# Performance work log

Hardware: AMD Instinct MI355X
Metric: run time of the kernel (lower is better)

## Reference

```python
import math
import jax, jax.numpy as jnp
import numpy as np

BS, T, D_MODEL, H = 4, 1024, 1024, 16
D_K = D_MODEL // H


def setup_inputs() -> dict:
    key = jax.random.key(0)
    ks = jax.random.split(key, 16)
    s = 0.02  # weight init scale
    return {
        "q": jax.random.normal(ks[0], (BS, T, D_MODEL), jnp.float32),
        "k": jax.random.normal(ks[1], (BS, T, D_MODEL), jnp.float32),
        "v": jax.random.normal(ks[2], (BS, T, D_MODEL), jnp.float32),
        "pos_emb": jax.random.normal(ks[3], (1, T, D_MODEL), jnp.float32),
        "mask": jnp.ones((BS, T, T), jnp.int32),
        "Wq": jax.random.normal(ks[4], (D_MODEL, D_MODEL), jnp.float32) * s,
        "bq": jax.random.normal(ks[5], (D_MODEL,), jnp.float32) * s,
        "Wk": jax.random.normal(ks[6], (D_MODEL, D_MODEL), jnp.float32) * s,
        "bk": jax.random.normal(ks[7], (D_MODEL,), jnp.float32) * s,
        "Wv": jax.random.normal(ks[8], (D_MODEL, D_MODEL), jnp.float32) * s,
        "bv": jax.random.normal(ks[9], (D_MODEL,), jnp.float32) * s,
        "Wp": jax.random.normal(ks[10], (D_MODEL, D_MODEL), jnp.float32) * s,
        "pos_bias_u": jax.random.normal(ks[11], (H, D_K), jnp.float32) * s,
        "pos_bias_v": jax.random.normal(ks[12], (H, D_K), jnp.float32) * s,
        "Wo": jax.random.normal(ks[13], (D_MODEL, D_MODEL), jnp.float32) * s,
        "bo": jax.random.normal(ks[14], (D_MODEL,), jnp.float32) * s,
    }


def rel_shift(x):
    # x: [b, h, T, P]; Transformer-XL relative shift via pad+reshape
    b, h, t, p = x.shape
    x = jnp.pad(x, ((0, 0), (0, 0), (0, 0), (1, 0)))  # [b,h,T,P+1]
    x = x.reshape(b, h, p + 1, t)[:, :, 1:, :]
    return x.reshape(b, h, t, p)


def reference(q, k, v, pos_emb, mask, Wq, bq, Wk, bk, Wv, bv, Wp,
              pos_bias_u, pos_bias_v, Wo, bo):
    bs, t, d_model = q.shape
    h, d_k = pos_bias_u.shape
    # projections (torch Linear: x @ W.T + b)
    qh = (q @ Wq.T + bq).reshape(bs, t, h, d_k)                      # [b,t,h,d]
    kh = (k @ Wk.T + bk).reshape(bs, t, h, d_k).transpose(0, 2, 1, 3)  # [b,h,s,d]
    vh = (v @ Wv.T + bv).reshape(bs, t, h, d_k).transpose(0, 2, 1, 3)  # [b,h,s,d]
    p = (pos_emb @ Wp.T).reshape(pos_emb.shape[0], -1, h, d_k).transpose(0, 2, 1, 3)  # [1,h,P,d]
    q_u = (qh + pos_bias_u).transpose(0, 2, 1, 3)  # [b,h,t,d]
    q_v = (qh + pos_bias_v).transpose(0, 2, 1, 3)  # [b,h,t,d]
    matrix_ac = jnp.einsum('bhtd,bhsd->bhts', q_u, kh)
    matrix_bd = jnp.einsum('bhtd,hpd->bhtp', q_v, p[0])
    matrix_bd = rel_shift(matrix_bd)
    scores = (matrix_ac + matrix_bd) / math.sqrt(d_k)
    m = mask[:, None, :, :]  # broadcast over heads
    attn = jax.nn.softmax(jnp.where(m == 0, jnp.float32(-10000.0), scores), axis=-1)
    out_h = jnp.einsum('bhts,bhsd->bhtd', attn, vh)
    concat = out_h.transpose(0, 2, 1, 3).reshape(bs, t, d_model)
    output = concat @ Wo.T + bo
    return (output, attn)
```

## Files before the change

### kernel.cpp

```cpp
#include <hip/hip_runtime.h>

typedef _Float16 f16;
typedef __attribute__((ext_vector_type(8))) _Float16 f16x8;
typedef __attribute__((ext_vector_type(4))) float f32x4;

#define LDK 40


__device__ __forceinline__ void stage_f32(const float* __restrict__ src, int ld, f16* dst) {
    int t = threadIdx.x;
    int row = t >> 2;
    int c0 = (t & 3) * 8;
    const float* p = src + (size_t)row * ld + c0;
    float4 u = *(const float4*)p;
    float4 w = *(const float4*)(p + 4);
    f16x8 h;
    h[0] = (f16)u.x; h[1] = (f16)u.y; h[2] = (f16)u.z; h[3] = (f16)u.w;
    h[4] = (f16)w.x; h[5] = (f16)w.y; h[6] = (f16)w.z; h[7] = (f16)w.w;
    *(f16x8*)(dst + row * LDK + c0) = h;
}

__device__ __forceinline__ void stage_f16g(const f16* __restrict__ src, int ld, f16* dst) {
    int t = threadIdx.x;
    int row = t >> 2;
    int c0 = (t & 3) * 8;
    *(f16x8*)(dst + row * LDK + c0) = *(const f16x8*)(src + (size_t)row * ld + c0);
}

__device__ __forceinline__ void stage_vT(const f16* __restrict__ src, f16* dst) {
    int t = threadIdx.x;
    int s = t >> 3;
    int d0 = (t & 7) * 8;
    f16x8 h = *(const f16x8*)(src + (size_t)s * 64 + d0);
#pragma unroll
    for (int j = 0; j < 8; ++j) dst[(d0 + j) * LDK + s] = h[j];
}


__device__ __forceinline__ void mma_step(const f16* As, const f16* Bs, int m_off, int n_off,
                                         f32x4 acc[2][2]) {
    int lane = threadIdx.x & 63;
    int r = lane & 15;
    int kq = (lane >> 4) * 8;
    f16x8 a0 = *(const f16x8*)(As + (m_off + r) * LDK + kq);
    f16x8 a1 = *(const f16x8*)(As + (m_off + 16 + r) * LDK + kq);
    f16x8 b0 = *(const f16x8*)(Bs + (n_off + r) * LDK + kq);
    f16x8 b1 = *(const f16x8*)(Bs + (n_off + 16 + r) * LDK + kq);
    acc[0][0] = __builtin_amdgcn_mfma_f32_16x16x32_f16(a0, b0, acc[0][0], 0, 0, 0);
    acc[0][1] = __builtin_amdgcn_mfma_f32_16x16x32_f16(a0, b1, acc[0][1], 0, 0, 0);
    acc[1][0] = __builtin_amdgcn_mfma_f32_16x16x32_f16(a1, b0, acc[1][0], 0, 0, 0);
    acc[1][1] = __builtin_amdgcn_mfma_f32_16x16x32_f16(a1, b1, acc[1][1], 0, 0, 0);
}

#define GEMM_PROLOGUE()                                         \
    __shared__ f16 As[64 * LDK];                                \
    __shared__ f16 Bs[64 * LDK];                                \
    const int w = threadIdx.x >> 6;                             \
    const int m_off = (w & 1) * 32, n_off = (w >> 1) * 32;      \
    const int lane = threadIdx.x & 63;                          \
    f32x4 zero = {0.f, 0.f, 0.f, 0.f};                          \
    f32x4 acc[2][2] = {{zero, zero}, {zero, zero}};

template <int MODE>
__global__ __launch_bounds__(256) void proj_gemm(
    const float* __restrict__ A, const float* __restrict__ W,
    const float* __restrict__ bias, const float* __restrict__ pbu,
    const float* __restrict__ pbv, f16* __restrict__ o1, f16* __restrict__ o2) {
    GEMM_PROLOGUE();
    const int m0 = blockIdx.y * 64;
    const int n0 = blockIdx.x * 64;
    for (int k0 = 0; k0 < 1024; k0 += 32) {
        stage_f32(A + (size_t)m0 * 1024 + k0, 1024, As);
        stage_f32(W + (size_t)n0 * 1024 + k0, 1024, Bs);
        __syncthreads();
        mma_step(As, Bs, m_off, n_off, acc);
        __syncthreads();
    }
#pragma unroll
    for (int mt = 0; mt < 2; ++mt)
#pragma unroll
        for (int nt = 0; nt < 2; ++nt)
#pragma unroll
            for (int rr = 0; rr < 4; ++rr) {
                int m = m0 + m_off + mt * 16 + (lane >> 4) * 4 + rr;
                int n = n0 + n_off + nt * 16 + (lane & 15);
                float vv = acc[mt][nt][rr];
                if (MODE == 2) {
                    int h = n >> 6, d = n & 63;
                    o1[((size_t)h * 1024 + m) * 64 + d] = (f16)vv;
                } else {
                    float base = vv + bias[n];
                    int b = m >> 10, t = m & 1023, h = n >> 6, d = n & 63;
                    size_t idx = ((size_t)((b * 16 + h) * 1024 + t)) * 64 + d;
                    if (MODE == 0) {
                        o1[idx] = (f16)(base + pbu[n]);
                        o2[idx] = (f16)(base + pbv[n]);
                    } else {
                        o1[idx] = (f16)base;
                    }
                }
            }
}

__global__ __launch_bounds__(256) void bd_gemm(const f16* __restrict__ qv,
                                               const f16* __restrict__ p,
                                               f16* __restrict__ bds) {
    GEMM_PROLOGUE();
    const int bh = blockIdx.z;
    const int h = bh & 15;
    const int m0 = blockIdx.y * 64, n0 = blockIdx.x * 64;
    const f16* Ab = qv + (size_t)bh * 65536;
    const f16* Bb = p + (size_t)h * 65536;
    for (int k0 = 0; k0 < 64; k0 += 32) {
        stage_f16g(Ab + (size_t)m0 * 64 + k0, 64, As);
        stage_f16g(Bb + (size_t)n0 * 64 + k0, 64, Bs);
        __syncthreads();
        mma_step(As, Bs, m_off, n_off, acc);
        __syncthreads();
    }
    f16* B0 = bds + (size_t)bh * 1048576;
#pragma unroll
    for (int mt = 0; mt < 2; ++mt)
#pragma unroll
        for (int nt = 0; nt < 2; ++nt)
#pragma unroll
            for (int rr = 0; rr < 4; ++rr) {
                int r = m0 + m_off + mt * 16 + (lane >> 4) * 4 + rr;
                int c = n0 + n_off + nt * 16 + (lane & 15);
                float vv = acc[mt][nt][rr];
                if (c >= 1023 - r) {
                    B0[(size_t)r * 1024 + (c + r - 1023)] = (f16)vv;
                } else if (r >= 1) {
                    B0[(size_t)(r - 1) * 1024 + (c + r + 1)] = (f16)vv;
                }
            }
}

__global__ __launch_bounds__(256) void ac_gemm(const f16* __restrict__ qu,
                                               const f16* __restrict__ kh,
                                               f16* __restrict__ bds) {
    GEMM_PROLOGUE();
    const int bh = blockIdx.z;
    const int m0 = blockIdx.y * 64, n0 = blockIdx.x * 64;
    const f16* Ab = qu + (size_t)bh * 65536;
    const f16* Bb = kh + (size_t)bh * 65536;
    for (int k0 = 0; k0 < 64; k0 += 32) {
        stage_f16g(Ab + (size_t)m0 * 64 + k0, 64, As);
        stage_f16g(Bb + (size_t)n0 * 64 + k0, 64, Bs);
        __syncthreads();
        mma_step(As, Bs, m_off, n_off, acc);
        __syncthreads();
    }
#pragma unroll
    for (int mt = 0; mt < 2; ++mt)
#pragma unroll
        for (int nt = 0; nt < 2; ++nt)
#pragma unroll
            for (int rr = 0; rr < 4; ++rr) {
                int i = m0 + m_off + mt * 16 + (lane >> 4) * 4 + rr;
                int j = n0 + n_off + nt * 16 + (lane & 15);
                size_t idx = (size_t)bh * 1048576 + (size_t)i * 1024 + j;
                float bdv = (j == i + 1) ? 0.f : (float)bds[idx];
                bds[idx] = (f16)((acc[mt][nt][rr] + bdv) * 0.125f);
            }
}

__global__ __launch_bounds__(256) void softmax_k(const f16* __restrict__ sp,
                                                 const int* __restrict__ mask,
                                                 float* __restrict__ attn) {
    const int row = blockIdx.x;
    const int bh = row >> 10, t = row & 1023;
    const int b = bh >> 4;
    const f16* s = sp + (size_t)row * 1024;
    const int* mk = mask + ((size_t)b * 1024 + t) * 1024;
    const int tid = threadIdx.x;
    float vals[4];
    float mx = -1e30f;
#pragma unroll
    for (int ii = 0; ii < 4; ++ii) {
        int c = tid + ii * 256;
        float v = (float)s[c];
        if (mk[c] == 0) v = -10000.0f;
        vals[ii] = v;
        mx = fmaxf(mx, v);
    }
#pragma unroll
    for (int off = 32; off > 0; off >>= 1) mx = fmaxf(mx, __shfl_xor(mx, off));
    __shared__ float red[4], red2[4];
    if ((tid & 63) == 0) red[tid >> 6] = mx;
    __syncthreads();
    mx = fmaxf(fmaxf(red[0], red[1]), fmaxf(red[2], red[3]));
    float sum = 0.f, e[4];
#pragma unroll
    for (int ii = 0; ii < 4; ++ii) {
        e[ii] = __expf(vals[ii] - mx);
        sum += e[ii];
    }
#pragma unroll
    for (int off = 32; off > 0; off >>= 1) sum += __shfl_xor(sum, off);
    if ((tid & 63) == 0) red2[tid >> 6] = sum;
    __syncthreads();
    sum = red2[0] + red2[1] + red2[2] + red2[3];
    float inv = 1.f / sum;
    float* arow = attn + (size_t)row * 1024;
#pragma unroll
    for (int ii = 0; ii < 4; ++ii) arow[tid + ii * 256] = e[ii] * inv;
}

__global__ __launch_bounds__(256) void pv_gemm(const float* __restrict__ attn,
                                               const f16* __restrict__ vh,
                                               f16* __restrict__ oh) {
    GEMM_PROLOGUE();
    const int bh = blockIdx.z;
    const int b = bh >> 4, h = bh & 15;
    const int m0 = blockIdx.y * 64;
    const float* Ab = attn + (size_t)bh * 1048576;
    const f16* Bb = vh + (size_t)bh * 65536;
    for (int k0 = 0; k0 < 1024; k0 += 32) {
        stage_f32(Ab + (size_t)m0 * 1024 + k0, 1024, As);
        stage_vT(Bb + (size_t)k0 * 64, Bs);
        __syncthreads();
        mma_step(As, Bs, m_off, n_off, acc);
        __syncthreads();
    }
#pragma unroll
    for (int mt = 0; mt < 2; ++mt)
#pragma unroll
        for (int nt = 0; nt < 2; ++nt)
#pragma unroll
            for (int rr = 0; rr < 4; ++rr) {
                int t = m0 + m_off + mt * 16 + (lane >> 4) * 4 + rr;
                int d = n_off + nt * 16 + (lane & 15);
                oh[((size_t)(b * 1024 + t)) * 1024 + h * 64 + d] =
                    (f16)acc[mt][nt][rr];
            }
}

__global__ __launch_bounds__(256) void out_gemm(const f16* __restrict__ A,
                                                const float* __restrict__ W,
                                                const float* __restrict__ bias,
                                                float* __restrict__ out) {
    GEMM_PROLOGUE();
    const int m0 = blockIdx.y * 64;
    const int n0 = blockIdx.x * 64;
    for (int k0 = 0; k0 < 1024; k0 += 32) {
        stage_f16g(A + (size_t)m0 * 1024 + k0, 1024, As);
        stage_f32(W + (size_t)n0 * 1024 + k0, 1024, Bs);
        __syncthreads();
        mma_step(As, Bs, m_off, n_off, acc);
        __syncthreads();
    }
#pragma unroll
    for (int mt = 0; mt < 2; ++mt)
#pragma unroll
        for (int nt = 0; nt < 2; ++nt)
#pragma unroll
            for (int rr = 0; rr < 4; ++rr) {
                int m = m0 + m_off + mt * 16 + (lane >> 4) * 4 + rr;
                int n = n0 + n_off + nt * 16 + (lane & 15);
                out[(size_t)m * 1024 + n] = acc[mt][nt][rr] + bias[n];
            }
}

extern "C" void kernel_launch(void* const* d_in, const int* in_sizes, int n_in,
                              void* d_out, int out_size, void* d_ws, size_t ws_size,
                              hipStream_t stream) {
    (void)in_sizes; (void)n_in; (void)out_size; (void)ws_size;
    const float* q   = (const float*)d_in[0];
    const float* k   = (const float*)d_in[1];
    const float* v   = (const float*)d_in[2];
    const float* pe  = (const float*)d_in[3];
    const int*   msk = (const int*)d_in[4];
    const float* Wq  = (const float*)d_in[5];
    const float* bq  = (const float*)d_in[6];
    const float* Wk  = (const float*)d_in[7];
    const float* bk  = (const float*)d_in[8];
    const float* Wv  = (const float*)d_in[9];
    const float* bv  = (const float*)d_in[10];
    const float* Wp  = (const float*)d_in[11];
    const float* pbu = (const float*)d_in[12];
    const float* pbv = (const float*)d_in[13];
    const float* Wo  = (const float*)d_in[14];
    const float* bo  = (const float*)d_in[15];

    char* ws = (char*)d_ws;
    f16* q_u = (f16*)(ws + 0);
    f16* q_v = (f16*)(ws + 8388608);
    f16* kh  = (f16*)(ws + 16777216);
    f16* vh  = (f16*)(ws + 25165824);
    f16* pp  = (f16*)(ws + 33554432);
    f16* bds = (f16*)(ws + 35651584);
    f16* oh  = (f16*)(ws + 169869312);

    float* out  = (float*)d_out;
    float* attn = out + 4194304;

    dim3 blk(256);
    proj_gemm<0><<<dim3(16, 64), blk, 0, stream>>>(q, Wq, bq, pbu, pbv, q_u, q_v);
    proj_gemm<1><<<dim3(16, 64), blk, 0, stream>>>(k, Wk, bk, nullptr, nullptr, kh, nullptr);
    proj_gemm<1><<<dim3(16, 64), blk, 0, stream>>>(v, Wv, bv, nullptr, nullptr, vh, nullptr);
    proj_gemm<2><<<dim3(16, 16), blk, 0, stream>>>(pe, Wp, nullptr, nullptr, nullptr, pp, nullptr);
    bd_gemm<<<dim3(16, 16, 64), blk, 0, stream>>>(q_v, pp, bds);
    ac_gemm<<<dim3(16, 16, 64), blk, 0, stream>>>(q_u, kh, bds);
    softmax_k<<<dim3(65536), blk, 0, stream>>>(bds, msk, attn);
    pv_gemm<<<dim3(1, 16, 64), blk, 0, stream>>>(attn, vh, oh);
    out_gemm<<<dim3(16, 64), blk, 0, stream>>>(oh, Wo, bo, out);
}
```

Before: 746.0 us.

## Pre-convert inputs to fp16, batch QKV projections, fuse softmax with PV GEMM

A single conversion kernel now turns all fp32 inputs and weights into fp16 once, so the GEMMs stage fp16 directly instead of converting inside every K-loop. The three Q/K/V projections run as one launch over a z dimension. Softmax and the P·V GEMM are merged into one kernel: it computes per-row max and sum, then recomputes the probabilities, writes the fp32 attention output, and feeds fp16 probabilities straight into the MFMA. This removes the re-read of the 256MB fp32 attn tensor. The trade-off is extra conversion traffic, reading the scores twice, and fewer blocks (1024) for the fused kernel.

Result: faster. 703.8 us (-5.6%).

```diff
diff --git a/kernel.cpp b/kernel.cpp
--- a/kernel.cpp
+++ b/kernel.cpp
@@ -6,19 +6,6 @@
 
 #define LDK 40
 
-
-__device__ __forceinline__ void stage_f32(const float* __restrict__ src, int ld, f16* dst) {
-    int t = threadIdx.x;
-    int row = t >> 2;
-    int c0 = (t & 3) * 8;
-    const float* p = src + (size_t)row * ld + c0;
-    float4 u = *(const float4*)p;
-    float4 w = *(const float4*)(p + 4);
-    f16x8 h;
-    h[0] = (f16)u.x; h[1] = (f16)u.y; h[2] = (f16)u.z; h[3] = (f16)u.w;
-    h[4] = (f16)w.x; h[5] = (f16)w.y; h[6] = (f16)w.z; h[7] = (f16)w.w;
-    *(f16x8*)(dst + row * LDK + c0) = h;
-}
 
 __device__ __forceinline__ void stage_f16g(const f16* __restrict__ src, int ld, f16* dst) {
     int t = threadIdx.x;
@@ -61,17 +48,82 @@
     f32x4 zero = {0.f, 0.f, 0.f, 0.f};                          \
     f32x4 acc[2][2] = {{zero, zero}, {zero, zero}};
 
-template <int MODE>
-__global__ __launch_bounds__(256) void proj_gemm(
-    const float* __restrict__ A, const float* __restrict__ W,
-    const float* __restrict__ bias, const float* __restrict__ pbu,
-    const float* __restrict__ pbv, f16* __restrict__ o1, f16* __restrict__ o2) {
+__global__ __launch_bounds__(256) void cvt_all(
+    const float* __restrict__ q, const float* __restrict__ k, const float* __restrict__ v,
+    const float* __restrict__ pe, const float* __restrict__ Wq, const float* __restrict__ Wk,
+    const float* __restrict__ Wv, const float* __restrict__ Wp, const float* __restrict__ Wo,
+    f16* __restrict__ dst) {
+    const int seg = blockIdx.y;
+    const float* srcs[9] = {q, k, v, pe, Wq, Wk, Wv, Wp, Wo};
+    const int sz = (seg < 3) ? 4194304 : 1048576;
+    const size_t off = (seg < 3) ? (size_t)seg * 4194304
+                                 : (size_t)12582912 + (size_t)(seg - 3) * 1048576;
+    const size_t i0 = ((size_t)blockIdx.x * 256 + threadIdx.x) * 16;
+    if (i0 >= (size_t)sz) return;
+    const float* s = srcs[seg] + i0;
+    f16* d = dst + off + i0;
+#pragma unroll
+    for (int half = 0; half < 2; ++half) {
+        float4 u = *(const float4*)(s + half * 8);
+        float4 w = *(const float4*)(s + half * 8 + 4);
+        f16x8 h;
+        h[0] = (f16)u.x; h[1] = (f16)u.y; h[2] = (f16)u.z; h[3] = (f16)u.w;
+        h[4] = (f16)w.x; h[5] = (f16)w.y; h[6] = (f16)w.z; h[7] = (f16)w.w;
+        *(f16x8*)(d + half * 8) = h;
+    }
+}
+
+__global__ __launch_bounds__(256) void proj_qkv(
+    const f16* __restrict__ qf, const f16* __restrict__ kf, const f16* __restrict__ vf,
+    const f16* __restrict__ Wqf, const f16* __restrict__ Wkf, const f16* __restrict__ Wvf,
+    const float* __restrict__ bq, const float* __restrict__ bk, const float* __restrict__ bv,
+    const float* __restrict__ pbu, const float* __restrict__ pbv,
+    f16* __restrict__ q_u, f16* __restrict__ q_v, f16* __restrict__ kh,
+    f16* __restrict__ vh) {
+    GEMM_PROLOGUE();
+    const int z = blockIdx.z;
+    const f16* A = (z == 0) ? qf : (z == 1) ? kf : vf;
+    const f16* W = (z == 0) ? Wqf : (z == 1) ? Wkf : Wvf;
+    const float* bias = (z == 0) ? bq : (z == 1) ? bk : bv;
+    const int m0 = blockIdx.y * 64, n0 = blockIdx.x * 64;
+    for (int k0 = 0; k0 < 1024; k0 += 32) {
+        stage_f16g(A + (size_t)m0 * 1024 + k0, 1024, As);
+        stage_f16g(W + (size_t)n0 * 1024 + k0, 1024, Bs);
+        __syncthreads();
+        mma_step(As, Bs, m_off, n_off, acc);
+        __syncthreads();
+    }
+#pragma unroll
+    for (int mt = 0; mt < 2; ++mt)
+#pragma unroll
+        for (int nt = 0; nt < 2; ++nt)
+#pragma unroll
+            for (int rr = 0; rr < 4; ++rr) {
+                int m = m0 + m_off + mt * 16 + (lane >> 4) * 4 + rr;
+                int n = n0 + n_off + nt * 16 + (lane & 15);
+                float base = acc[mt][nt][rr] + bias[n];
+                int b = m >> 10, t = m & 1023, h = n >> 6, d = n & 63;
+                size_t idx = ((size_t)((b * 16 + h) * 1024 + t)) * 64 + d;
+                if (z == 0) {
+                    q_u[idx] = (f16)(base + pbu[n]);
+                    q_v[idx] = (f16)(base + pbv[n]);
+                } else if (z == 1) {
+                    kh[idx] = (f16)base;
+                } else {
+                    vh[idx] = (f16)base;
+                }
+            }
+}
+
+__global__ __launch_bounds__(256) void proj_p(const f16* __restrict__ A,
+                                              const f16* __restrict__ W,
+                                              f16* __restrict__ o1) {
     GEMM_PROLOGUE();
     const int m0 = blockIdx.y * 64;
     const int n0 = blockIdx.x * 64;
     for (int k0 = 0; k0 < 1024; k0 += 32) {
-        stage_f32(A + (size_t)m0 * 1024 + k0, 1024, As);
-        stage_f32(W + (size_t)n0 * 1024 + k0, 1024, Bs);
+        stage_f16g(A + (size_t)m0 * 1024 + k0, 1024, As);
+        stage_f16g(W + (size_t)n0 * 1024 + k0, 1024, Bs);
         __syncthreads();
         mma_step(As, Bs, m_off, n_off, acc);
         __syncthreads();
@@ -84,21 +136,8 @@
             for (int rr = 0; rr < 4; ++rr) {
                 int m = m0 + m_off + mt * 16 + (lane >> 4) * 4 + rr;
                 int n = n0 + n_off + nt * 16 + (lane & 15);
-                float vv = acc[mt][nt][rr];
-                if (MODE == 2) {
-                    int h = n >> 6, d = n & 63;
-                    o1[((size_t)h * 1024 + m) * 64 + d] = (f16)vv;
-                } else {
-                    float base = vv + bias[n];
-                    int b = m >> 10, t = m & 1023, h = n >> 6, d = n & 63;
-                    size_t idx = ((size_t)((b * 16 + h) * 1024 + t)) * 64 + d;
-                    if (MODE == 0) {
-                        o1[idx] = (f16)(base + pbu[n]);
-                        o2[idx] = (f16)(base + pbv[n]);
-                    } else {
-                        o1[idx] = (f16)base;
-                    }
-                }
+                int h = n >> 6, d = n & 63;
+                o1[((size_t)h * 1024 + m) * 64 + d] = (f16)acc[mt][nt][rr];
             }
 }
 
@@ -165,71 +204,99 @@
             }
 }
 
-__global__ __launch_bounds__(256) void softmax_k(const f16* __restrict__ sp,
-                                                 const int* __restrict__ mask,
-                                                 float* __restrict__ attn) {
-    const int row = blockIdx.x;
-    const int bh = row >> 10, t = row & 1023;
-    const int b = bh >> 4;
-    const f16* s = sp + (size_t)row * 1024;
-    const int* mk = mask + ((size_t)b * 1024 + t) * 1024;
-    const int tid = threadIdx.x;
-    float vals[4];
-    float mx = -1e30f;
-#pragma unroll
-    for (int ii = 0; ii < 4; ++ii) {
-        int c = tid + ii * 256;
-        float v = (float)s[c];
-        if (mk[c] == 0) v = -10000.0f;
-        vals[ii] = v;
-        mx = fmaxf(mx, v);
-    }
-#pragma unroll
-    for (int off = 32; off > 0; off >>= 1) mx = fmaxf(mx, __shfl_xor(mx, off));
-    __shared__ float red[4], red2[4];
-    if ((tid & 63) == 0) red[tid >> 6] = mx;
+__global__ __launch_bounds__(256) void softmax_pv(const f16* __restrict__ scores,
+                                                  const int* __restrict__ mask,
+                                                  const f16* __restrict__ vh,
+                                                  float* __restrict__ attn,
+                                                  f16* __restrict__ oh) {
+    const int bh = blockIdx.y;
+    const int i0 = blockIdx.x * 64;
+    const int b = bh >> 4, h = bh & 15;
+    const f16* S = scores + (size_t)bh * 1048576 + (size_t)i0 * 1024;
+    const int* MK = mask + ((size_t)b * 1024 + i0) * 1024;
+    __shared__ float s_max[64], s_invl[64];
+
+    const int w = threadIdx.x >> 6;
+    const int lane = threadIdx.x & 63;
+
+    for (int rr = 0; rr < 16; ++rr) {
+        int r = w * 16 + rr;
+        const f16* srow = S + (size_t)r * 1024 + lane * 16;
+        const int* mrow = MK + (size_t)r * 1024 + lane * 16;
+        f16x8 a0 = *(const f16x8*)srow;
+        f16x8 a1 = *(const f16x8*)(srow + 8);
+        int4 m0 = *(const int4*)mrow;
+        int4 m1 = *(const int4*)(mrow + 4);
+        int4 m2 = *(const int4*)(mrow + 8);
+        int4 m3 = *(const int4*)(mrow + 12);
+        int mks[16] = {m0.x, m0.y, m0.z, m0.w, m1.x, m1.y, m1.z, m1.w,
+                       m2.x, m2.y, m2.z, m2.w, m3.x, m3.y, m3.z, m3.w};
+        float vals[16];
+        float mx = -1e30f;
+#pragma unroll
+        for (int j = 0; j < 16; ++j) {
+            float v = (j < 8) ? (float)a0[j] : (float)a1[j - 8];
+            if (mks[j] == 0) v = -10000.0f;
+            vals[j] = v;
+            mx = fmaxf(mx, v);
+        }
+#pragma unroll
+        for (int off = 32; off > 0; off >>= 1) mx = fmaxf(mx, __shfl_xor(mx, off));
+        float sum = 0.f;
+#pragma unroll
+        for (int j = 0; j < 16; ++j) sum += __expf(vals[j] - mx);
+#pragma unroll
+        for (int off = 32; off > 0; off >>= 1) sum += __shfl_xor(sum, off);
+        if (lane == 0) {
+            s_max[r] = mx;
+            s_invl[r] = 1.f / sum;
+        }
+    }
     __syncthreads();
-    mx = fmaxf(fmaxf(red[0], red[1]), fmaxf(red[2], red[3]));
-    float sum = 0.f, e[4];
-#pragma unroll
-    for (int ii = 0; ii < 4; ++ii) {
-        e[ii] = __expf(vals[ii] - mx);
-        sum += e[ii];
-    }
-#pragma unroll
-    for (int off = 32; off > 0; off >>= 1) sum += __shfl_xor(sum, off);
-    if ((tid & 63) == 0) red2[tid >> 6] = sum;
-    __syncthreads();
-    sum = red2[0] + red2[1] + red2[2] + red2[3];
-    float inv = 1.f / sum;
-    float* arow = attn + (size_t)row * 1024;
-#pragma unroll
-    for (int ii = 0; ii < 4; ++ii) arow[tid + ii * 256] = e[ii] * inv;
-}
-
-__global__ __launch_bounds__(256) void pv_gemm(const float* __restrict__ attn,
-                                               const f16* __restrict__ vh,
-                                               f16* __restrict__ oh) {
-    GEMM_PROLOGUE();
-    const int bh = blockIdx.z;
-    const int b = bh >> 4, h = bh & 15;
-    const int m0 = blockIdx.y * 64;
-    const float* Ab = attn + (size_t)bh * 1048576;
-    const f16* Bb = vh + (size_t)bh * 65536;
-    for (int k0 = 0; k0 < 1024; k0 += 32) {
-        stage_f32(Ab + (size_t)m0 * 1024 + k0, 1024, As);
-        stage_vT(Bb + (size_t)k0 * 64, Bs);
-        __syncthreads();
-        mma_step(As, Bs, m_off, n_off, acc);
-        __syncthreads();
-    }
-#pragma unroll
-    for (int mt = 0; mt < 2; ++mt)
-#pragma unroll
-        for (int nt = 0; nt < 2; ++nt)
-#pragma unroll
-            for (int rr = 0; rr < 4; ++rr) {
-                int t = m0 + m_off + mt * 16 + (lane >> 4) * 4 + rr;
+
+    __shared__ f16 As[64 * LDK];
+    __shared__ f16 Bs[64 * LDK];
+    const int m_off = (w & 1) * 32, n_off = (w >> 1) * 32;
+    f32x4 zero = {0.f, 0.f, 0.f, 0.f};
+    f32x4 acc[2][2] = {{zero, zero}, {zero, zero}};
+    const int r2 = threadIdx.x >> 2;
+    const int c2 = (threadIdx.x & 3) * 8;
+    const f16* Vb = vh + (size_t)bh * 65536;
+    float* arow = attn + (size_t)bh * 1048576 + (size_t)(i0 + r2) * 1024 + c2;
+
+    for (int j0 = 0; j0 < 1024; j0 += 32) {
+        f16x8 sv = *(const f16x8*)(S + (size_t)r2 * 1024 + j0 + c2);
+        const int* mp = MK + (size_t)r2 * 1024 + j0 + c2;
+        int4 mk0 = *(const int4*)mp;
+        int4 mk1 = *(const int4*)(mp + 4);
+        int mks[8] = {mk0.x, mk0.y, mk0.z, mk0.w, mk1.x, mk1.y, mk1.z, mk1.w};
+        float mx = s_max[r2], il = s_invl[r2];
+        f16x8 pv;
+        float po[8];
+#pragma unroll
+        for (int j = 0; j < 8; ++j) {
+            float s = (float)sv[j];
+            if (mks[j] == 0) s = -10000.0f;
+            float p = __expf(s - mx) * il;
+            po[j] = p;
+            pv[j] = (f16)p;
+        }
+        *(float4*)(arow + j0) = {po[0], po[1], po[2], po[3]};
+        *(float4*)(arow + j0 + 4) = {po[4], po[5], po[6], po[7]};
+        *(f16x8*)(As + r2 * LDK + c2) = pv;
+        stage_vT(Vb + (size_t)j0 * 64, Bs);
+        __syncthreads();
+        mma_step(As, Bs, m_off, n_off, acc);
+        __syncthreads();
+    }
+
+#pragma unroll
+    for (int mt = 0; mt < 2; ++mt)
+#pragma unroll
+        for (int nt = 0; nt < 2; ++nt)
+#pragma unroll
+            for (int rr = 0; rr < 4; ++rr) {
+                int t = i0 + m_off + mt * 16 + (lane >> 4) * 4 + rr;
                 int d = n_off + nt * 16 + (lane & 15);
                 oh[((size_t)(b * 1024 + t)) * 1024 + h * 64 + d] =
                     (f16)acc[mt][nt][rr];
@@ -237,7 +304,7 @@
 }
 
 __global__ __launch_bounds__(256) void out_gemm(const f16* __restrict__ A,
-                                                const float* __restrict__ W,
+                                                const f16* __restrict__ W,
                                                 const float* __restrict__ bias,
                                                 float* __restrict__ out) {
     GEMM_PROLOGUE();
@@ -245,7 +312,7 @@
     const int n0 = blockIdx.x * 64;
     for (int k0 = 0; k0 < 1024; k0 += 32) {
         stage_f16g(A + (size_t)m0 * 1024 + k0, 1024, As);
-        stage_f32(W + (size_t)n0 * 1024 + k0, 1024, Bs);
+        stage_f16g(W + (size_t)n0 * 1024 + k0, 1024, Bs);
         __syncthreads();
         mma_step(As, Bs, m_off, n_off, acc);
         __syncthreads();
@@ -284,25 +351,35 @@
     const float* bo  = (const float*)d_in[15];
 
     char* ws = (char*)d_ws;
-    f16* q_u = (f16*)(ws + 0);
-    f16* q_v = (f16*)(ws + 8388608);
-    f16* kh  = (f16*)(ws + 16777216);
-    f16* vh  = (f16*)(ws + 25165824);
-    f16* pp  = (f16*)(ws + 33554432);
-    f16* bds = (f16*)(ws + 35651584);
-    f16* oh  = (f16*)(ws + 169869312);
+    f16* cvt = (f16*)(ws + 0);
+    f16* qf  = cvt;
+    f16* kf  = cvt + 4194304;
+    f16* vf  = cvt + 8388608;
+    f16* pef = cvt + 12582912;
+    f16* Wqf = cvt + 13631488;
+    f16* Wkf = cvt + 14680064;
+    f16* Wvf = cvt + 15728640;
+    f16* Wpf = cvt + 16777216;
+    f16* Wof = cvt + 17825792;
+
+    f16* q_u = (f16*)(ws + 37748736);
+    f16* q_v = (f16*)(ws + 46137344);
+    f16* kh  = (f16*)(ws + 54525952);
+    f16* vh  = (f16*)(ws + 62914560);
+    f16* pp  = (f16*)(ws + 71303168);
+    f16* bds = (f16*)(ws + 73400320);
+    f16* oh  = (f16*)(ws + 207618048);
 
     float* out  = (float*)d_out;
     float* attn = out + 4194304;
 
     dim3 blk(256);
-    proj_gemm<0><<<dim3(16, 64), blk, 0, stream>>>(q, Wq, bq, pbu, pbv, q_u, q_v);
-    proj_gemm<1><<<dim3(16, 64), blk, 0, stream>>>(k, Wk, bk, nullptr, nullptr, kh, nullptr);
-    proj_gemm<1><<<dim3(16, 64), blk, 0, stream>>>(v, Wv, bv, nullptr, nullptr, vh, nullptr);
-    proj_gemm<2><<<dim3(16, 16), blk, 0, stream>>>(pe, Wp, nullptr, nullptr, nullptr, pp, nullptr);
+    cvt_all<<<dim3(1024, 9), blk, 0, stream>>>(q, k, v, pe, Wq, Wk, Wv, Wp, Wo, cvt);
+    proj_qkv<<<dim3(16, 64, 3), blk, 0, stream>>>(qf, kf, vf, Wqf, Wkf, Wvf, bq, bk, bv,
+                                                  pbu, pbv, q_u, q_v, kh, vh);
+    proj_p<<<dim3(16, 16), blk, 0, stream>>>(pef, Wpf, pp);
     bd_gemm<<<dim3(16, 16, 64), blk, 0, stream>>>(q_v, pp, bds);
     ac_gemm<<<dim3(16, 16, 64), blk, 0, stream>>>(q_u, kh, bds);
-    softmax_k<<<dim3(65536), blk, 0, stream>>>(bds, msk, attn);
-    pv_gemm<<<dim3(1, 16, 64), blk, 0, stream>>>(attn, vh, oh);
-    out_gemm<<<dim3(16, 64), blk, 0, stream>>>(oh, Wo, bo, out);
-}
+    softmax_pv<<<dim3(16, 64), blk, 0, stream>>>(bds, msk, vh, attn, oh);
+    out_gemm<<<dim3(16, 64), blk, 0, stream>>>(oh, Wof, bo, out);
+}
```
